# Kernel optimization log

Hardware: AMD Instinct MI355X
Metric: run time of the kernel (lower is better)

The kernel has to match this reference:

```python
import jax, jax.numpy as jnp
import numpy as np

TEMPERATURE = 34.0
PAD = 1  # kernel_size // 2

def setup_inputs() -> dict:
    key = jax.random.key(0)
    ks = jax.random.split(key, 5)
    B, C, H, W = 32, 256, 56, 56
    K, O, I, kh = 4, 256, 256, 3
    hidden = int(C * 0.25) + 1  # 65
    return {
        "x": jax.random.normal(ks[0], (B, C, H, W), jnp.float32),
        "fc1_w": jax.random.normal(ks[1], (hidden, C), jnp.float32) * (2.0 / C) ** 0.5,
        "fc2_w": jax.random.normal(ks[2], (K, hidden), jnp.float32) * (2.0 / hidden) ** 0.5,
        "fc2_b": jnp.zeros((K,), jnp.float32),
        "weight": jax.random.normal(ks[3], (K, O, I, kh, kh), jnp.float32) * (2.0 / (I * kh * kh)) ** 0.5,
        "bias": jnp.zeros((K, O), jnp.float32),
    }

def reference(x, fc1_w, fc2_w, fc2_b, weight, bias):
    # attention2d: global avg pool -> 1x1 conv (fc1) -> relu -> 1x1 conv (fc2) -> softmax(logits/T)
    pooled = x.mean(axis=(2, 3))                      # [B, C]
    h = jax.nn.relu(pooled @ fc1_w.T)                 # [B, hidden]
    logits = h @ fc2_w.T + fc2_b                      # [B, K]
    att = jax.nn.softmax(logits / TEMPERATURE, axis=1)
    # aggregate per-sample conv weights/bias over K kernel banks
    agg_w = jnp.einsum('bk,koihw->boihw', att, weight)  # [B, O, I, kh, kw]
    agg_b = att @ bias                                  # [B, O]
    # per-sample conv (torch emulates via groups=B): vmap over batch
    def conv_one(xi, wi):
        return jax.lax.conv_general_dilated(
            xi[None], wi, window_strides=(1, 1),
            padding=((PAD, PAD), (PAD, PAD)),
            dimension_numbers=('NCHW', 'OIHW', 'NCHW'))[0]
    out = jax.vmap(conv_one)(x, agg_w)                 # [B, O, H, W]
    return out + agg_b[:, :, None, None]
```

## Files before the change

### kernel.cpp

```cpp
#include <hip/hip_runtime.h>


typedef short bf16x8 __attribute__((ext_vector_type(8)));
typedef float f32x16 __attribute__((ext_vector_type(16)));

__device__ __forceinline__ unsigned short f2bf(float f) {
  unsigned int u = __float_as_uint(f);
  return (unsigned short)((u + 0x7FFFu + ((u >> 16) & 1u)) >> 16);
}
__device__ __forceinline__ float bf2f(unsigned short h) {
  return __uint_as_float(((unsigned int)h) << 16);
}

__global__ void xcast_k(const float* __restrict__ x, unsigned short* __restrict__ xb,
                        float* __restrict__ pooled) {
  __shared__ __align__(16) unsigned short tile[64 * 260];
  int b = blockIdx.y;
  int hw0 = blockIdx.x * 64;
  int t = threadIdx.x;
  int lane = t & 63, wq = t >> 6;
#pragma unroll 8
  for (int it = 0; it < 64; ++it) {
    int c = it * 4 + wq;
    float v = x[((size_t)(b * 256 + c)) * 3136 + hw0 + lane];
    tile[lane * 260 + c] = f2bf(v);
  }
  __syncthreads();
  int c4 = lane * 4;
#pragma unroll
  for (int it = 0; it < 16; ++it) {
    int hl = it * 4 + wq;
    ushort4 v = *(const ushort4*)&tile[hl * 260 + c4];
    *(ushort4*)&xb[((size_t)(b * 3136 + hw0 + hl)) * 256 + c4] = v;
  }
  float s = 0.f;
#pragma unroll 16
  for (int hl = 0; hl < 64; ++hl) s += bf2f(tile[hl * 260 + t]);
  atomicAdd(&pooled[b * 256 + t], s * (1.0f / 3136.0f));
}

__global__ void att_k(const float* __restrict__ pooled, const float* __restrict__ fc1,
                      const float* __restrict__ fc2w, const float* __restrict__ fc2b,
                      const float* __restrict__ bias, float* __restrict__ att,
                      float* __restrict__ aggb) {
  int b = blockIdx.x, t = threadIdx.x;
  __shared__ float p[256];
  __shared__ float h[65];
  __shared__ float a4[4];
  for (int i = t; i < 256; i += 64) p[i] = pooled[b * 256 + i];
  __syncthreads();
  for (int j = t; j < 65; j += 64) {
    float s = 0.f;
    for (int c = 0; c < 256; ++c) s += p[c] * fc1[j * 256 + c];
    h[j] = fmaxf(s, 0.f);
  }
  __syncthreads();
  if (t == 0) {
    float lg[4];
    for (int k = 0; k < 4; ++k) {
      float s = fc2b[k];
      for (int j = 0; j < 65; ++j) s += h[j] * fc2w[k * 65 + j];
      lg[k] = s * (1.0f / 34.0f);
    }
    float m = fmaxf(fmaxf(lg[0], lg[1]), fmaxf(lg[2], lg[3]));
    float e0 = expf(lg[0] - m), e1 = expf(lg[1] - m), e2 = expf(lg[2] - m), e3 = expf(lg[3] - m);
    float inv = 1.0f / (e0 + e1 + e2 + e3);
    a4[0] = e0 * inv; a4[1] = e1 * inv; a4[2] = e2 * inv; a4[3] = e3 * inv;
    for (int k = 0; k < 4; ++k) att[b * 4 + k] = a4[k];
  }
  __syncthreads();
  for (int o = t; o < 256; o += 64) {
    float s = 0.f;
    for (int k = 0; k < 4; ++k) s += a4[k] * bias[k * 256 + o];
    aggb[b * 256 + o] = s;
  }
}

__global__ void aggw_k(const float* __restrict__ weight, const float* __restrict__ att,
                       unsigned short* __restrict__ aggw) {
  __shared__ float wl[4 * 2304];
  int o = blockIdx.x, t = threadIdx.x;
  for (int k = 0; k < 4; ++k)
    for (int idx = t; idx < 2304; idx += 256)
      wl[k * 2304 + idx] = weight[((size_t)(k * 256 + o)) * 2304 + idx];
  __syncthreads();
  int ot = o >> 7, ol = o & 127, ic = t >> 4, il = t & 15;
  int b0 = blockIdx.y * 8;
  for (int b = b0; b < b0 + 8; ++b) {
    float a0 = att[b * 4 + 0], a1 = att[b * 4 + 1], a2 = att[b * 4 + 2], a3 = att[b * 4 + 3];
    size_t base = ((size_t)((b * 2 + ot) * 16 + ic)) * (9 * 2048) + ol * 16 + il;
#pragma unroll
    for (int r = 0; r < 9; ++r) {
      float s = a0 * wl[t * 9 + r] + a1 * wl[2304 + t * 9 + r] +
                a2 * wl[4608 + t * 9 + r] + a3 * wl[6912 + t * 9 + r];
      aggw[base + r * 2048] = f2bf(s);
    }
  }
}

#define XBUF 16384

__global__ __launch_bounds__(256, 2) void conv_k(const unsigned short* __restrict__ xb,
                                                 const unsigned short* __restrict__ aggw,
                                                 const float* __restrict__ aggb,
                                                 float* __restrict__ out) {
  __shared__ __align__(16) unsigned char lds[2 * XBUF];
  const int t = threadIdx.x;
  const int wid = t >> 6, lane = t & 63, l31 = lane & 31, q = lane >> 5;
  const int wo = wid >> 1, wn = wid & 1;

  int id = blockIdx.x;
  int wgid = (id & 7) * 104 + (id >> 3);
  int bn = wgid % 13;
  int rest = wgid / 13;
  int b = rest >> 1, bo = rest & 1;

  const int o0 = bo * 128;
  const int n0 = bn * 256;
  const int h0 = n0 / 56;

  int bbase[4], nn[4], swz[4][3];
#pragma unroll
  for (int nf = 0; nf < 4; ++nf) {
    int n = n0 + wn * 128 + nf * 32 + l31;
    int h = n / 56, w = n - h * 56;
    nn[nf] = n;
    bbase[nf] = ((h - h0) * 64 + w) * 32 + q * 16;
#pragma unroll
    for (int dw = 0; dw < 3; ++dw) swz[nf][dw] = ((w + dw) & 7) << 4;
  }
  int aoff[2];
#pragma unroll
  for (int mf = 0; mf < 2; ++mf) aoff[mf] = (wo * 64 + mf * 32 + l31) * 32 + q * 16;

  int xsrc[4], xdst[4];
#pragma unroll
  for (int j = 0; j < 4; ++j) {
    int idx = j * 256 + t;
    int pos = idx >> 1, sub = idx & 1;
    int row = pos >> 6, col = pos & 63;
    int hg = h0 - 1 + row, wg = col - 1;
    bool valid = (col >= 1 && col <= 56 && hg >= 0 && hg < 56);
    xsrc[j] = valid ? ((hg * 56 + wg) * 512 + sub * 16) : -1;
    xdst[j] = (idx * 16) ^ ((pos & 7) << 4);
  }

  f32x16 acc[2][4];
#pragma unroll
  for (int i = 0; i < 2; ++i)
#pragma unroll
    for (int j = 0; j < 4; ++j)
#pragma unroll
      for (int e = 0; e < 16; ++e) acc[i][j][e] = 0.f;

  const char* xb_b = (const char*)xb + (size_t)b * 3136 * 512;
  const char* ag_c = (const char*)aggw + (size_t)rest * 589824;

#pragma unroll
  for (int j = 0; j < 4; ++j) {
    uint4 v = make_uint4(0u, 0u, 0u, 0u);
    if (xsrc[j] >= 0) v = *(const uint4*)(xb_b + xsrc[j]);
    *(uint4*)(lds + xdst[j]) = v;
  }
  __syncthreads();

  int cur = 0;
  for (int ic = 0; ic < 16; ++ic) {
    uint4 nv[4];
    const bool more = (ic + 1 < 16);
    if (more) {
#pragma unroll
      for (int j = 0; j < 4; ++j) {
        uint4 v = make_uint4(0u, 0u, 0u, 0u);
        if (xsrc[j] >= 0) v = *(const uint4*)(xb_b + xsrc[j] + (ic + 1) * 32);
        nv[j] = v;
      }
    }
    const unsigned char* xlds = lds + cur * XBUF;
    const char* agc = ag_c + (size_t)ic * 36864;
#pragma unroll
    for (int r = 0; r < 9; ++r) {
      const int dh = r / 3, dw = r % 3;
      bf16x8 a0 = *(const bf16x8*)(agc + r * 4096 + aoff[0]);
      bf16x8 a1 = *(const bf16x8*)(agc + r * 4096 + aoff[1]);
#pragma unroll
      for (int nf = 0; nf < 4; ++nf) {
        bf16x8 bb = *(const bf16x8*)(xlds + ((bbase[nf] + dh * 2048 + dw * 32) ^ swz[nf][dw]));
        acc[0][nf] = __builtin_amdgcn_mfma_f32_32x32x16_bf16(a0, bb, acc[0][nf], 0, 0, 0);
        acc[1][nf] = __builtin_amdgcn_mfma_f32_32x32x16_bf16(a1, bb, acc[1][nf], 0, 0, 0);
      }
    }
    if (more) {
      unsigned char* dst = lds + (cur ^ 1) * XBUF;
#pragma unroll
      for (int j = 0; j < 4; ++j) *(uint4*)(dst + xdst[j]) = nv[j];
      __syncthreads();
    }
    cur ^= 1;
  }

#pragma unroll
  for (int mf = 0; mf < 2; ++mf) {
#pragma unroll
    for (int reg = 0; reg < 16; ++reg) {
      int o = o0 + wo * 64 + mf * 32 + (reg & 3) + 8 * (reg >> 2) + 4 * q;
      float ab = aggb[b * 256 + o];
      float* op = out + ((size_t)(b * 256 + o)) * 3136;
#pragma unroll
      for (int nf = 0; nf < 4; ++nf) {
        if (nn[nf] < 3136) op[nn[nf]] = acc[mf][nf][reg] + ab;
      }
    }
  }
}

extern "C" void kernel_launch(void* const* d_in, const int* in_sizes, int n_in,
                              void* d_out, int out_size, void* d_ws, size_t ws_size,
                              hipStream_t stream) {
  const float* x      = (const float*)d_in[0];
  const float* fc1    = (const float*)d_in[1];
  const float* fc2w   = (const float*)d_in[2];
  const float* fc2b   = (const float*)d_in[3];
  const float* weight = (const float*)d_in[4];
  const float* bias   = (const float*)d_in[5];
  float* out = (float*)d_out;

  char* ws = (char*)d_ws;
  float* pooled         = (float*)(ws);
  float* att            = (float*)(ws + 32768);
  float* aggb           = (float*)(ws + 33280);
  unsigned short* aggw  = (unsigned short*)(ws + 66048);
  unsigned short* xb    = (unsigned short*)(ws + 66048 + 37748736);

  hipMemsetAsync(pooled, 0, 32768, stream);
  xcast_k<<<dim3(49, 32), 256, 0, stream>>>(x, xb, pooled);
  att_k<<<32, 64, 0, stream>>>(pooled, fc1, fc2w, fc2b, bias, att, aggb);
  aggw_k<<<dim3(256, 4), 256, 0, stream>>>(weight, att, aggw);
  conv_k<<<832, 256, 0, stream>>>(xb, aggw, aggb, out);
}
```

Baseline: 232.5 us.

## Stage conv inputs and weights into LDS via direct global-to-LDS loads

The conv kernel now uses global_load_lds DMA to fill LDS. It double-buffers the input tile and also stages the per-channel-chunk aggregated weights in a swizzled LDS region, where before the weights were read from global memory directly in the MFMA loop. Out-of-range input positions read from a zeroed scratch buffer instead of branching, and MFMA issue is wrapped in s_setprio. The xcast kernel switches to float4 loads. The extra 36 KB of dynamic LDS per block and the additional barrier per iteration could limit occupancy and overlap.

```diff
diff --git a/kernel.cpp b/kernel.cpp
--- a/kernel.cpp
+++ b/kernel.cpp
@@ -12,20 +12,38 @@
   return __uint_as_float(((unsigned int)h) << 16);
 }
 
+__device__ __forceinline__ int invswz(int S) {
+  int b7 = (S >> 7) & 1;
+  int b6 = ((S >> 6) & 1) ^ b7;
+  int b5 = ((S >> 5) & 1) ^ b6;
+  int b4 = ((S >> 4) & 1) ^ b5;
+  return (S & ~0x70) | (b4 << 4) | (b5 << 5) | (b6 << 6);
+}
+
+typedef const __attribute__((address_space(1))) unsigned int* gas_t;
+typedef __attribute__((address_space(3))) unsigned int* las_t;
+__device__ __forceinline__ void dma16(const void* g, unsigned lds_addr) {
+  __builtin_amdgcn_global_load_lds((gas_t)g, (las_t)(size_t)lds_addr, 16, 0, 0);
+}
+
 __global__ void xcast_k(const float* __restrict__ x, unsigned short* __restrict__ xb,
                         float* __restrict__ pooled) {
-  __shared__ __align__(16) unsigned short tile[64 * 260];
+  __shared__ unsigned short tile[64 * 260];
   int b = blockIdx.y;
   int hw0 = blockIdx.x * 64;
   int t = threadIdx.x;
+  int p = t & 15, g = t >> 4;
+#pragma unroll
+  for (int i = 0; i < 16; ++i) {
+    int c = g + 16 * i;
+    float4 v = *(const float4*)(x + ((size_t)(b * 256 + c)) * 3136 + hw0 + p * 4);
+    tile[(p * 4 + 0) * 260 + c] = f2bf(v.x);
+    tile[(p * 4 + 1) * 260 + c] = f2bf(v.y);
+    tile[(p * 4 + 2) * 260 + c] = f2bf(v.z);
+    tile[(p * 4 + 3) * 260 + c] = f2bf(v.w);
+  }
+  __syncthreads();
   int lane = t & 63, wq = t >> 6;
-#pragma unroll 8
-  for (int it = 0; it < 64; ++it) {
-    int c = it * 4 + wq;
-    float v = x[((size_t)(b * 256 + c)) * 3136 + hw0 + lane];
-    tile[lane * 260 + c] = f2bf(v);
-  }
-  __syncthreads();
   int c4 = lane * 4;
 #pragma unroll
   for (int it = 0; it < 16; ++it) {
@@ -99,12 +117,15 @@
 }
 
 #define XBUF 16384
+#define AOFF 32768
 
 __global__ __launch_bounds__(256, 2) void conv_k(const unsigned short* __restrict__ xb,
                                                  const unsigned short* __restrict__ aggw,
                                                  const float* __restrict__ aggb,
+                                                 const float* __restrict__ zerobuf,
                                                  float* __restrict__ out) {
-  __shared__ __align__(16) unsigned char lds[2 * XBUF];
+  extern __shared__ unsigned char lds[];
+  const unsigned ldsbase = (unsigned)(size_t)&lds[0];
   const int t = threadIdx.x;
   const int wid = t >> 6, lane = t & 63, l31 = lane & 31, q = lane >> 5;
   const int wo = wid >> 1, wn = wid & 1;
@@ -129,21 +150,28 @@
 #pragma unroll
     for (int dw = 0; dw < 3; ++dw) swz[nf][dw] = ((w + dw) & 7) << 4;
   }
-  int aoff[2];
-#pragma unroll
-  for (int mf = 0; mf < 2; ++mf) aoff[mf] = (wo * 64 + mf * 32 + l31) * 32 + q * 16;
-
-  int xsrc[4], xdst[4];
+  int abase[2];
+#pragma unroll
+  for (int mf = 0; mf < 2; ++mf) {
+    int ol = wo * 64 + mf * 32 + l31;
+    abase[mf] = AOFF + ((ol * 32 + q * 16) ^ ((ol & 7) << 4));
+  }
+
+  const char* xb_b = (const char*)xb + (size_t)b * 3136 * 512;
+  const char* ag_c = (const char*)aggw + (size_t)rest * 589824;
+
+  const char* xg[4];
 #pragma unroll
   for (int j = 0; j < 4; ++j) {
-    int idx = j * 256 + t;
-    int pos = idx >> 1, sub = idx & 1;
+    int S = (j * 256 + t) * 16;
+    int L = invswz(S);
+    int pos = L >> 5, sub = (L >> 4) & 1;
     int row = pos >> 6, col = pos & 63;
     int hg = h0 - 1 + row, wg = col - 1;
     bool valid = (col >= 1 && col <= 56 && hg >= 0 && hg < 56);
-    xsrc[j] = valid ? ((hg * 56 + wg) * 512 + sub * 16) : -1;
-    xdst[j] = (idx * 16) ^ ((pos & 7) << 4);
-  }
+    xg[j] = valid ? (xb_b + (size_t)(hg * 56 + wg) * 512 + sub * 16) : (const char*)zerobuf;
+  }
+  const char* aL = ag_c + invswz(t * 16);
 
   f32x16 acc[2][4];
 #pragma unroll
@@ -153,47 +181,45 @@
 #pragma unroll
       for (int e = 0; e < 16; ++e) acc[i][j][e] = 0.f;
 
-  const char* xb_b = (const char*)xb + (size_t)b * 3136 * 512;
-  const char* ag_c = (const char*)aggw + (size_t)rest * 589824;
-
-#pragma unroll
-  for (int j = 0; j < 4; ++j) {
-    uint4 v = make_uint4(0u, 0u, 0u, 0u);
-    if (xsrc[j] >= 0) v = *(const uint4*)(xb_b + xsrc[j]);
-    *(uint4*)(lds + xdst[j]) = v;
-  }
+#pragma unroll
+  for (int j = 0; j < 4; ++j) dma16(xg[j], ldsbase + j * 4096 + wid * 1024);
+#pragma unroll
+  for (int j = 0; j < 9; ++j) dma16(aL + j * 4096, ldsbase + AOFF + j * 4096 + wid * 1024);
   __syncthreads();
 
   int cur = 0;
   for (int ic = 0; ic < 16; ++ic) {
-    uint4 nv[4];
-    const bool more = (ic + 1 < 16);
-    if (more) {
-#pragma unroll
-      for (int j = 0; j < 4; ++j) {
-        uint4 v = make_uint4(0u, 0u, 0u, 0u);
-        if (xsrc[j] >= 0) v = *(const uint4*)(xb_b + xsrc[j] + (ic + 1) * 32);
-        nv[j] = v;
-      }
-    }
     const unsigned char* xlds = lds + cur * XBUF;
-    const char* agc = ag_c + (size_t)ic * 36864;
 #pragma unroll
     for (int r = 0; r < 9; ++r) {
       const int dh = r / 3, dw = r % 3;
-      bf16x8 a0 = *(const bf16x8*)(agc + r * 4096 + aoff[0]);
-      bf16x8 a1 = *(const bf16x8*)(agc + r * 4096 + aoff[1]);
-#pragma unroll
-      for (int nf = 0; nf < 4; ++nf) {
-        bf16x8 bb = *(const bf16x8*)(xlds + ((bbase[nf] + dh * 2048 + dw * 32) ^ swz[nf][dw]));
-        acc[0][nf] = __builtin_amdgcn_mfma_f32_32x32x16_bf16(a0, bb, acc[0][nf], 0, 0, 0);
-        acc[1][nf] = __builtin_amdgcn_mfma_f32_32x32x16_bf16(a1, bb, acc[1][nf], 0, 0, 0);
+      bf16x8 a0 = *(const bf16x8*)(lds + abase[0] + r * 4096);
+      bf16x8 a1 = *(const bf16x8*)(lds + abase[1] + r * 4096);
+      bf16x8 b0 = *(const bf16x8*)(xlds + ((bbase[0] + dh * 2048 + dw * 32) ^ swz[0][dw]));
+      bf16x8 b1 = *(const bf16x8*)(xlds + ((bbase[1] + dh * 2048 + dw * 32) ^ swz[1][dw]));
+      bf16x8 b2 = *(const bf16x8*)(xlds + ((bbase[2] + dh * 2048 + dw * 32) ^ swz[2][dw]));
+      bf16x8 b3 = *(const bf16x8*)(xlds + ((bbase[3] + dh * 2048 + dw * 32) ^ swz[3][dw]));
+      __builtin_amdgcn_s_setprio(1);
+      acc[0][0] = __builtin_amdgcn_mfma_f32_32x32x16_bf16(a0, b0, acc[0][0], 0, 0, 0);
+      acc[0][1] = __builtin_amdgcn_mfma_f32_32x32x16_bf16(a0, b1, acc[0][1], 0, 0, 0);
+      acc[0][2] = __builtin_amdgcn_mfma_f32_32x32x16_bf16(a0, b2, acc[0][2], 0, 0, 0);
+      acc[0][3] = __builtin_amdgcn_mfma_f32_32x32x16_bf16(a0, b3, acc[0][3], 0, 0, 0);
+      acc[1][0] = __builtin_amdgcn_mfma_f32_32x32x16_bf16(a1, b0, acc[1][0], 0, 0, 0);
+      acc[1][1] = __builtin_amdgcn_mfma_f32_32x32x16_bf16(a1, b1, acc[1][1], 0, 0, 0);
+      acc[1][2] = __builtin_amdgcn_mfma_f32_32x32x16_bf16(a1, b2, acc[1][2], 0, 0, 0);
+      acc[1][3] = __builtin_amdgcn_mfma_f32_32x32x16_bf16(a1, b3, acc[1][3], 0, 0, 0);
+      __builtin_amdgcn_s_setprio(0);
+      if (r == 0 && ic + 1 < 16) {
+#pragma unroll
+        for (int j = 0; j < 4; ++j)
+          dma16(xg[j] + (ic + 1) * 32, ldsbase + (cur ^ 1) * XBUF + j * 4096 + wid * 1024);
       }
     }
-    if (more) {
-      unsigned char* dst = lds + (cur ^ 1) * XBUF;
-#pragma unroll
-      for (int j = 0; j < 4; ++j) *(uint4*)(dst + xdst[j]) = nv[j];
+    __syncthreads();
+    if (ic + 1 < 16) {
+#pragma unroll
+      for (int j = 0; j < 9; ++j)
+        dma16(aL + (size_t)(ic + 1) * 36864 + j * 4096, ldsbase + AOFF + j * 4096 + wid * 1024);
       __syncthreads();
     }
     cur ^= 1;
@@ -232,9 +258,13 @@
   unsigned short* aggw  = (unsigned short*)(ws + 66048);
   unsigned short* xb    = (unsigned short*)(ws + 66048 + 37748736);
 
+  hipFuncSetAttribute(reinterpret_cast<const void*>(conv_k),
+                      hipFuncAttributeMaxDynamicSharedMemorySize, 2 * XBUF + 36864);
+
   hipMemsetAsync(pooled, 0, 32768, stream);
   xcast_k<<<dim3(49, 32), 256, 0, stream>>>(x, xb, pooled);
   att_k<<<32, 64, 0, stream>>>(pooled, fc1, fc2w, fc2b, bias, att, aggb);
+  hipMemsetAsync(pooled, 0, 1024, stream);
   aggw_k<<<dim3(256, 4), 256, 0, stream>>>(weight, att, aggw);
-  conv_k<<<832, 256, 0, stream>>>(xb, aggw, aggb, out);
-}
+  conv_k<<<832, 256, 2 * XBUF + 36864, stream>>>(xb, aggw, aggb, (const float*)pooled, out);
+}
```

New measurement: 232.7 us. No clear change (+0.1%).
